# Optimization experiments

Hardware: AMD Instinct MI355X
Metric: run time of the kernel (lower is better)

Reference implementation:

```python
import jax, jax.numpy as jnp
import numpy as np

B, L, C, H = 4, 2048, 1024, 16
D = C // H  # head dim = 64


def setup_inputs() -> dict:
    key = jax.random.key(0)
    ks = jax.random.split(key, 7)
    x = jax.random.normal(ks[0], (B, L, C), dtype=jnp.float32)
    Wqkv = jax.random.normal(ks[1], (C, 3 * C), dtype=jnp.float32) * 0.02
    bqkv = jnp.zeros((3 * C,), dtype=jnp.float32)
    gamma_q = jnp.ones((H, D), dtype=jnp.float32)
    gamma_k = jnp.ones((H, D), dtype=jnp.float32)
    Wout = jax.random.normal(ks[2], (C, C), dtype=jnp.float32) * 0.02
    bout = jnp.zeros((C,), dtype=jnp.float32)
    return {"x": x, "Wqkv": Wqkv, "bqkv": bqkv, "gamma_q": gamma_q,
            "gamma_k": gamma_k, "Wout": Wout, "bout": bout}


def _multihead_rms_norm(t, gamma):
    # SparseMultiHeadRMSNorm: L2-normalize last dim (F.normalize), * gamma * sqrt(D)
    norm = jnp.maximum(jnp.linalg.norm(t, axis=-1, keepdims=True), 1e-12)
    return (t / norm) * gamma * jnp.sqrt(jnp.float32(D))


def reference(x, Wqkv, bqkv, gamma_q, gamma_k, Wout, bout):
    # qkv projection: [B,L,C] -> [B,L,3,H,D]
    qkv = (x @ Wqkv + bqkv).reshape(B, L, 3, H, D)
    q, k, v = qkv[:, :, 0], qkv[:, :, 1], qkv[:, :, 2]
    # qk rms norm (gamma broadcasts over [B,L,H,D])
    q = _multihead_rms_norm(q, gamma_q)
    k = _multihead_rms_norm(k, gamma_k)
    # full scaled dot product attention within each grid (batch element)
    scale = 1.0 / jnp.sqrt(jnp.float32(D))
    scores = jnp.einsum('bqhd,bkhd->bhqk', q, k) * scale
    attn = jax.nn.softmax(scores, axis=-1)
    h = jnp.einsum('bhqk,bkhd->bqhd', attn, v).reshape(B, L, C)
    return h @ Wout + bout
```

## Files before the change

### kernel.cpp

```cpp
#include <hip/hip_runtime.h>
#include <math.h>

#define BB 4
#define LL 2048
#define CC 1024
#define HH 16
#define DD 64
#define MM (BB * LL)

typedef float f32x4 __attribute__((ext_vector_type(4)));
typedef short short8 __attribute__((ext_vector_type(8)));
typedef unsigned short ushort_t;
typedef unsigned long long u64_t;

#define MFMA_BF16(A, B, C) __builtin_amdgcn_mfma_f32_16x16x32_bf16(A, B, C, 0, 0, 0)

#define QSCALE 0.180336880f

__device__ __forceinline__ unsigned short f2bf(float x) {
    unsigned int u = __float_as_uint(x);
    u += 0x7fffu + ((u >> 16) & 1u);
    return (unsigned short)(u >> 16);
}
__device__ __forceinline__ float bf2f(unsigned short h) {
    return __uint_as_float(((unsigned int)h) << 16);
}

__device__ __forceinline__ unsigned pack_bf2(float a, float b) {
#if __has_builtin(__builtin_amdgcn_perm)
    return __builtin_amdgcn_perm(__float_as_uint(b) + 0x8000u,
                                 __float_as_uint(a) + 0x8000u, 0x07060302u);
#else
    return ((__float_as_uint(b) + 0x8000u) & 0xFFFF0000u) |
           ((__float_as_uint(a) + 0x8000u) >> 16);
#endif
}

__device__ __forceinline__ float fast_exp2(float x) {
#if __has_builtin(__builtin_amdgcn_exp2f)
    return __builtin_amdgcn_exp2f(x);
#else
    return exp2f(x);
#endif
}

__global__ __launch_bounds__(256)
void round_bf16(const float* __restrict__ src, ushort_t* __restrict__ dst, int n)
{
    const int i = (blockIdx.x * 256 + threadIdx.x) * 8;
    if (i >= n) return;
    f32x4 a = *(const f32x4*)(src + i);
    f32x4 b = *(const f32x4*)(src + i + 4);
    short8 h;
#pragma unroll
    for (int j = 0; j < 4; ++j) {
        h[j]     = (short)f2bf(a[j]);
        h[4 + j] = (short)f2bf(b[j]);
    }
    *(short8*)(dst + i) = h;
}

__global__ __launch_bounds__(256)
void transp_hi(const float* __restrict__ W, ushort_t* __restrict__ Th,
               int K, int N)
{
    __shared__ float sT[64][65];
    const int k0 = blockIdx.y * 64, n0 = blockIdx.x * 64;
    const int tid = threadIdx.x;
    const int r = tid >> 2, c0 = (tid & 3) * 16;

    const float* wp = W + (size_t)(k0 + r) * N + n0 + c0;
#pragma unroll
    for (int u = 0; u < 4; ++u) {
        f32x4 v = *(const f32x4*)(wp + 4 * u);
        sT[r][c0 + 4 * u + 0] = v[0];
        sT[r][c0 + 4 * u + 1] = v[1];
        sT[r][c0 + 4 * u + 2] = v[2];
        sT[r][c0 + 4 * u + 3] = v[3];
    }
    __syncthreads();

    const int nn = tid >> 2, kk0 = (tid & 3) * 16;
    short8 h0, h1;
#pragma unroll
    for (int u = 0; u < 8; ++u) {
        h0[u] = (short)f2bf(sT[kk0 + u][nn]);
        h1[u] = (short)f2bf(sT[kk0 + 8 + u][nn]);
    }
    ushort_t* oh = Th + (size_t)(n0 + nn) * K + k0 + kk0;
    *(short8*)oh = h0; *(short8*)(oh + 8) = h1;
}

__global__ __launch_bounds__(256, 3)
void gemm_qkv(const ushort_t* __restrict__ Agh,
              const ushort_t* __restrict__ Bh,
              const float* __restrict__ bias,
              const float* __restrict__ gq, const float* __restrict__ gk,
              ushort_t* __restrict__ Qbh,
              ushort_t* __restrict__ Kh,
              ushort_t* __restrict__ Vth)
{
    __shared__ ushort_t smem[16384];
    ushort_t* sAh = smem;
    ushort_t* sBh = smem + 8192;

    const int K = CC, lda = CC, nbx = (3 * CC) / 128;

    const int nwg = gridDim.x;
    const int cpx = nwg >> 3;
    const int id  = blockIdx.x;
    const int swz = (id & 7) * cpx + (id >> 3);
    const int bx = swz % nbx, by = swz / nbx;
    const int m0 = by * 128, n0 = bx * 128;

    const int tid  = threadIdx.x;
    const int lane = tid & 63;
    const int wv   = tid >> 6;
    const int l4   = lane >> 4, l16 = lane & 15;
    const int wm   = wv >> 1,  wn  = wv & 1;

    const int r0  = tid >> 2;
    const int c0  = (tid & 3) * 16;
    const int ch0 = c0 >> 3;

    f32x4 acc[4][4];
#pragma unroll
    for (int i = 0; i < 4; ++i)
#pragma unroll
        for (int j = 0; j < 4; ++j) acc[i][j] = 0.f;

    for (int kt = 0; kt < K; kt += 64) {
        __syncthreads();
#pragma unroll
        for (int it = 0; it < 2; ++it) {
            const int row  = r0 + 64 * it;
            const int sA   = row & 7;
            const int base = row * 64;
            const int cA = ((ch0) ^ sA) * 8, cB = ((ch0 + 1) ^ sA) * 8;

            const ushort_t* ahp = Agh + (size_t)(m0 + row) * lda + kt + c0;
            *(short8*)&sAh[base + cA] = *(const short8*)(ahp);
            *(short8*)&sAh[base + cB] = *(const short8*)(ahp + 8);
            const ushort_t* bhp = Bh + (size_t)(n0 + row) * K + kt + c0;
            *(short8*)&sBh[base + cA] = *(const short8*)(bhp);
            *(short8*)&sBh[base + cB] = *(const short8*)(bhp + 8);
        }
        __syncthreads();

#pragma unroll
        for (int ks = 0; ks < 2; ++ks) {
            const int chf = (((ks << 2) | l4) ^ (l16 & 7)) * 8;
            short8 fbh[4];
#pragma unroll
            for (int j = 0; j < 4; ++j) {
                const int idx = (64 * wn + 16 * j + l16) * 64 + chf;
                fbh[j] = *(const short8*)&sBh[idx];
            }
#pragma unroll
            for (int i = 0; i < 4; ++i) {
                const int idx = (64 * wm + 16 * i + l16) * 64 + chf;
                short8 fah = *(const short8*)&sAh[idx];
#pragma unroll
                for (int j = 0; j < 4; ++j)
                    acc[i][j] = MFMA_BF16(fah, fbh[j], acc[i][j]);
            }
        }
    }

    const int region = n0 >> 10;
    float bv[4];
#pragma unroll
    for (int j = 0; j < 4; ++j) bv[j] = bias[n0 + 64 * wn + 16 * j + l16];
#pragma unroll
    for (int i = 0; i < 4; ++i)
#pragma unroll
        for (int j = 0; j < 4; ++j)
#pragma unroll
            for (int r = 0; r < 4; ++r) acc[i][j][r] += bv[j];

    const int b = m0 >> 11;

    if (region < 2) {
        const int hloc = ((n0 & 1023) >> 6) + wn;
        const float* g = (region == 0 ? gq : gk) + hloc * DD;
        float gv[4];
#pragma unroll
        for (int j = 0; j < 4; ++j) gv[j] = g[16 * j + l16];
#pragma unroll
        for (int i = 0; i < 4; ++i)
#pragma unroll
        for (int r = 0; r < 4; ++r) {
            float ss = 0.f;
#pragma unroll
            for (int j = 0; j < 4; ++j) ss += acc[i][j][r] * acc[i][j][r];
#pragma unroll
            for (int off = 1; off < 16; off <<= 1) ss += __shfl_xor(ss, off);
            const float s = 8.0f / fmaxf(sqrtf(ss), 1e-12f);
#pragma unroll
            for (int j = 0; j < 4; ++j) acc[i][j][r] *= s * gv[j];
        }

        if (region == 0) {
#pragma unroll
            for (int i = 0; i < 4; ++i)
#pragma unroll
            for (int r = 0; r < 4; ++r) {
                const int row = m0 + 64 * wm + 16 * i + 4 * l4 + r;
                ushort_t* op = Qbh + (size_t)row * CC + n0 + 64 * wn + l16;
#pragma unroll
                for (int j = 0; j < 4; ++j)
                    op[16 * j] = f2bf(acc[i][j][r] * QSCALE);
            }
        } else {
            const int hk = ((n0 - 1024) >> 6) + wn;
#pragma unroll
            for (int i = 0; i < 4; ++i)
#pragma unroll
            for (int r = 0; r < 4; ++r) {
                const int l = (m0 & 2047) + 64 * wm + 16 * i + 4 * l4 + r;
                const size_t base = ((size_t)(b * HH + hk) * LL + l) * DD + l16;
#pragma unroll
                for (int j = 0; j < 4; ++j)
                    Kh[base + 16 * j] = f2bf(acc[i][j][r]);
            }
        }
    } else {
        __syncthreads();
        ushort_t* vh = smem;
#pragma unroll
        for (int i = 0; i < 4; ++i)
#pragma unroll
        for (int r = 0; r < 4; ++r) {
            const int lr = 64 * wm + 16 * i + 4 * l4 + r;
#pragma unroll
            for (int j = 0; j < 4; ++j) {
                const int c = 64 * wn + 16 * j + l16;
                vh[lr * 128 + c] = f2bf(acc[i][j][r]);
            }
        }
        __syncthreads();
        const int c    = tid & 127;
        const int half = tid >> 7;
        const int hv   = ((n0 - 2048) >> 6) + (c >> 6);
        const int d    = c & 63;
        ushort_t* oh = Vth + ((size_t)(b * HH + hv) * DD + d) * LL + (m0 & 2047) + half * 64;
#pragma unroll
        for (int u = 0; u < 8; ++u) {
            const int l0 = half * 64 + u * 8;
            short8 hv8;
#pragma unroll
            for (int e = 0; e < 8; ++e)
                hv8[e] = (short)vh[(l0 + e) * 128 + c];
            *(short8*)&oh[u * 8] = hv8;
        }
    }
}

__global__ __launch_bounds__(256, 3)
void gemm_out1(const ushort_t* __restrict__ Ah,
               const ushort_t* __restrict__ Bh,
               const float* __restrict__ bias, float* __restrict__ Cg)
{
    __shared__ ushort_t sAh[8192];
    __shared__ ushort_t sBh[8192];

    const int K = CC, nbx = CC / 128;

    const int nwg = gridDim.x;
    const int cpx = nwg >> 3;
    const int id  = blockIdx.x;
    const int sw  = (id & 7) * cpx + (id >> 3);
    const int bx = sw % nbx, by = sw / nbx;
    const int m0 = by * 128, n0 = bx * 128;

    const int tid  = threadIdx.x;
    const int lane = tid & 63;
    const int wv   = tid >> 6;
    const int l4   = lane >> 4, l16 = lane & 15;
    const int wm   = wv >> 1,  wn  = wv & 1;

    const int r0  = tid >> 2;
    const int c0  = (tid & 3) * 16;
    const int ch0 = c0 >> 3;

    f32x4 acc[4][4];
#pragma unroll
    for (int i = 0; i < 4; ++i)
#pragma unroll
        for (int j = 0; j < 4; ++j) acc[i][j] = 0.f;

    for (int kt = 0; kt < K; kt += 64) {
        __syncthreads();
#pragma unroll
        for (int it = 0; it < 2; ++it) {
            const int row  = r0 + 64 * it;
            const int sA   = row & 7;
            const int base = row * 64;
            const int cA = ((ch0) ^ sA) * 8, cB = ((ch0 + 1) ^ sA) * 8;

            const ushort_t* ahp = Ah + (size_t)(m0 + row) * CC + kt + c0;
            *(short8*)&sAh[base + cA] = *(const short8*)(ahp);
            *(short8*)&sAh[base + cB] = *(const short8*)(ahp + 8);
            const ushort_t* bhp = Bh + (size_t)(n0 + row) * K + kt + c0;
            *(short8*)&sBh[base + cA] = *(const short8*)(bhp);
            *(short8*)&sBh[base + cB] = *(const short8*)(bhp + 8);
        }
        __syncthreads();

#pragma unroll
        for (int ks = 0; ks < 2; ++ks) {
            const int chf = (((ks << 2) | l4) ^ (l16 & 7)) * 8;
            short8 fbh[4];
#pragma unroll
            for (int j = 0; j < 4; ++j) {
                const int idx = (64 * wn + 16 * j + l16) * 64 + chf;
                fbh[j] = *(const short8*)&sBh[idx];
            }
#pragma unroll
            for (int i = 0; i < 4; ++i) {
                const int idx = (64 * wm + 16 * i + l16) * 64 + chf;
                short8 fah = *(const short8*)&sAh[idx];
#pragma unroll
                for (int j = 0; j < 4; ++j)
                    acc[i][j] = MFMA_BF16(fah, fbh[j], acc[i][j]);
            }
        }
    }

    float bv[4];
#pragma unroll
    for (int j = 0; j < 4; ++j) bv[j] = bias[n0 + 64 * wn + 16 * j + l16];
#pragma unroll
    for (int i = 0; i < 4; ++i)
#pragma unroll
    for (int r = 0; r < 4; ++r) {
        const int row = m0 + 64 * wm + 16 * i + 4 * l4 + r;
        float* cp = Cg + (size_t)row * CC + n0 + 64 * wn + l16;
#pragma unroll
        for (int j = 0; j < 4; ++j) cp[16 * j] = acc[i][j][r] + bv[j];
    }
}

__global__ __launch_bounds__(256, 3)
void flash9(const ushort_t* __restrict__ Qbh,
            const ushort_t* __restrict__ Kh,
            const ushort_t* __restrict__ Vth,
            ushort_t* __restrict__ Hb)
{
    __shared__ ushort_t sKh[4096], sVh[4096];
    __shared__ ushort_t sP[4][32 * 68];

    const int i    = blockIdx.x;
    const int xcd  = i & 7;
    const int slot = i >> 3;
    const int qt   = slot & 15;
    const int bh   = ((slot >> 4) << 3) | xcd;
    const int b    = bh >> 4, h = bh & 15;

    const int tid  = threadIdx.x;
    const int lane = tid & 63;
    const int wv   = tid >> 6;
    const int l4   = lane >> 4, l16 = lane & 15;

    short8 qh[2][2];
    const int qr0 = qt * 128 + wv * 32;
#pragma unroll
    for (int qf = 0; qf < 2; ++qf)
#pragma unroll
    for (int sl = 0; sl < 2; ++sl)
        qh[qf][sl] = *(const short8*)(Qbh + (size_t)(b * LL + qr0 + qf * 16 + l16) * CC
                                      + h * DD + sl * 32 + l4 * 8);

    short8 ones;
#pragma unroll
    for (int j = 0; j < 8; ++j) ones[j] = (short)0x3F80;

    f32x4 O[2][4];
    f32x4 acc_l[2];
#pragma unroll
    for (int qf = 0; qf < 2; ++qf) {
        acc_l[qf] = 0.f;
#pragma unroll
        for (int t = 0; t < 4; ++t) O[qf][t] = 0.f;
    }

    const int r_ = tid >> 2;
    const int c2 = (tid & 3) * 2;

    short8 stg[4];
    {
        const size_t kgb = ((size_t)bh * LL + r_) * DD + c2 * 8;
        const size_t vgb = ((size_t)bh * DD + r_) * LL + c2 * 8;
        stg[0] = *(const short8*)&Kh[kgb];  stg[1] = *(const short8*)&Kh[kgb + 8];
        stg[2] = *(const short8*)&Vth[vgb]; stg[3] = *(const short8*)&Vth[vgb + 8];
    }

    for (int kt = 0; kt < LL / 64; ++kt) {
        __syncthreads();
        {
            const int wr = r_ * 64, s = r_ & 7;
            const int cA = ((c2) ^ s) * 8, cB = ((c2 + 1) ^ s) * 8;
            *(short8*)&sKh[wr + cA] = stg[0];
            *(short8*)&sKh[wr + cB] = stg[1];
            *(short8*)&sVh[wr + cA] = stg[2];
            *(short8*)&sVh[wr + cB] = stg[3];
        }
        __syncthreads();
        if (kt + 1 < LL / 64) {
            const size_t kgb = ((size_t)bh * LL + (kt + 1) * 64 + r_) * DD + c2 * 8;
            const size_t vgb = ((size_t)bh * DD + r_) * LL + (kt + 1) * 64 + c2 * 8;
            stg[0] = *(const short8*)&Kh[kgb];  stg[1] = *(const short8*)&Kh[kgb + 8];
            stg[2] = *(const short8*)&Vth[vgb]; stg[3] = *(const short8*)&Vth[vgb + 8];
        }

        f32x4 S[2][4];
#pragma unroll
        for (int qf = 0; qf < 2; ++qf)
#pragma unroll
        for (int t = 0; t < 4; ++t) S[qf][t] = 0.f;

        __builtin_amdgcn_s_setprio(1);
#pragma unroll
        for (int t = 0; t < 4; ++t) {
            const int row = 16 * t + l16;
            const int swr = row & 7;
#pragma unroll
            for (int sl = 0; sl < 2; ++sl) {
                const int idx = row * 64 + (((sl << 2) | l4) ^ swr) * 8;
                short8 kh8 = *(const short8*)&sKh[idx];
#pragma unroll
                for (int qf = 0; qf < 2; ++qf)
                    S[qf][t] = MFMA_BF16(kh8, qh[qf][sl], S[qf][t]);
            }
        }
        __builtin_amdgcn_s_setprio(0);

#pragma unroll
        for (int qf = 0; qf < 2; ++qf)
#pragma unroll
        for (int t = 0; t < 4; ++t)
#pragma unroll
            for (int r = 0; r < 4; ++r)
                S[qf][t][r] = fast_exp2(S[qf][t][r]);

#pragma unroll
        for (int qf = 0; qf < 2; ++qf)
#pragma unroll
        for (int t = 0; t < 4; ++t) {
            unsigned lo = pack_bf2(S[qf][t][0], S[qf][t][1]);
            unsigned hi = pack_bf2(S[qf][t][2], S[qf][t][3]);
            const int widx = (qf * 16 + l16) * 68 + 16 * t + 4 * l4;
            *(u64_t*)&sP[wv][widx] = (u64_t)lo | ((u64_t)hi << 32);
        }
        asm volatile("s_waitcnt lgkmcnt(0)" ::: "memory");
        __builtin_amdgcn_sched_barrier(0);

        short8 pa[2][2];
#pragma unroll
        for (int qf = 0; qf < 2; ++qf)
#pragma unroll
        for (int sl = 0; sl < 2; ++sl) {
            const int ridx = (qf * 16 + l16) * 68 + sl * 32 + 8 * l4;
            union { u64_t q[2]; short8 s8; } u;
            u.q[0] = *(const u64_t*)&sP[wv][ridx];
            u.q[1] = *(const u64_t*)&sP[wv][ridx + 4];
            pa[qf][sl] = u.s8;
        }

        __builtin_amdgcn_s_setprio(1);
#pragma unroll
        for (int qf = 0; qf < 2; ++qf) {
            acc_l[qf] = MFMA_BF16(pa[qf][0], ones, acc_l[qf]);
            acc_l[qf] = MFMA_BF16(pa[qf][1], ones, acc_l[qf]);
        }
#pragma unroll
        for (int dt = 0; dt < 4; ++dt) {
            const int row = 16 * dt + l16;
            const int swr = row & 7;
#pragma unroll
            for (int sl = 0; sl < 2; ++sl) {
                const int idx = row * 64 + (((sl << 2) | l4) ^ swr) * 8;
                short8 vh8 = *(const short8*)&sVh[idx];
#pragma unroll
                for (int qf = 0; qf < 2; ++qf)
                    O[qf][dt] = MFMA_BF16(pa[qf][sl], vh8, O[qf][dt]);
            }
        }
        __builtin_amdgcn_s_setprio(0);
    }

#pragma unroll
    for (int qf = 0; qf < 2; ++qf) {
        f32x4 iv;
#pragma unroll
        for (int r = 0; r < 4; ++r) iv[r] = 1.0f / acc_l[qf][r];
#pragma unroll
        for (int r = 0; r < 4; ++r) {
            const int q = qr0 + qf * 16 + 4 * l4 + r;
            ushort_t* op = Hb + (size_t)(b * LL + q) * CC + h * DD + l16;
#pragma unroll
            for (int dt = 0; dt < 4; ++dt)
                op[16 * dt] = f2bf(O[qf][dt][r] * iv[r]);
        }
    }
}

#define Bb 128
#define Bn 128
#define BKG 8

__global__ __launch_bounds__(256)
void gemm_bias(const float* __restrict__ A, const float* __restrict__ B,
               const float* __restrict__ bias, float* __restrict__ C,
               int M, int N, int K, int lda, int ldb, int ldc)
{
    __shared__ float As[BKG][Bb];
    __shared__ float Bs[BKG][Bn];

    const int tid = threadIdx.x;
    const int m0 = blockIdx.y * Bb;
    const int n0 = blockIdx.x * Bn;
    const int ty = tid >> 4, tx = tid & 15;
    const int arow = tid >> 1, acol = (tid & 1) * 4;
    const int brow = tid >> 5, bcol = (tid & 31) * 4;

    const float* Ap = A + (size_t)(m0 + arow) * lda + acol;
    const float* Bp = B + (size_t)brow * ldb + n0 + bcol;

    float acc[8][8];
#pragma unroll
    for (int i = 0; i < 8; ++i)
#pragma unroll
        for (int j = 0; j < 8; ++j) acc[i][j] = 0.f;

    for (int k0 = 0; k0 < K; k0 += BKG) {
        float4 av = *(const float4*)(Ap + k0);
        float4 bv = *(const float4*)(Bp + (size_t)k0 * ldb);
        __syncthreads();
        As[acol + 0][arow] = av.x;
        As[acol + 1][arow] = av.y;
        As[acol + 2][arow] = av.z;
        As[acol + 3][arow] = av.w;
        *(float4*)&Bs[brow][bcol] = bv;
        __syncthreads();
#pragma unroll
        for (int kk = 0; kk < BKG; ++kk) {
            float a[8], bvv[8];
            *(float4*)&a[0] = *(const float4*)&As[kk][ty * 4];
            *(float4*)&a[4] = *(const float4*)&As[kk][64 + ty * 4];
            *(float4*)&bvv[0] = *(const float4*)&Bs[kk][tx * 4];
            *(float4*)&bvv[4] = *(const float4*)&Bs[kk][64 + tx * 4];
#pragma unroll
            for (int i = 0; i < 8; ++i)
#pragma unroll
                for (int j = 0; j < 8; ++j)
                    acc[i][j] = fmaf(a[i], bvv[j], acc[i][j]);
        }
    }
#pragma unroll
    for (int ih = 0; ih < 2; ++ih)
#pragma unroll
    for (int i = 0; i < 4; ++i) {
        const int m = m0 + ih * 64 + ty * 4 + i;
#pragma unroll
        for (int jh = 0; jh < 2; ++jh) {
            const int n = n0 + jh * 64 + tx * 4;
            float4 o;
            o.x = acc[ih*4+i][jh*4+0] + bias[n+0];
            o.y = acc[ih*4+i][jh*4+1] + bias[n+1];
            o.z = acc[ih*4+i][jh*4+2] + bias[n+2];
            o.w = acc[ih*4+i][jh*4+3] + bias[n+3];
            *(float4*)(C + (size_t)m * ldc + n) = o;
        }
    }
}

__global__ __launch_bounds__(256)
void rmsnorm_qk(float* __restrict__ qkv,
                const float* __restrict__ gq, const float* __restrict__ gk)
{
    const int gt    = blockIdx.x * 256 + threadIdx.x;
    const int lane  = gt & 63;
    const int wave  = gt >> 6;
    const int which = wave & 1;
    const int h     = (wave >> 1) & (HH - 1);
    const int bl    = wave >> 5;

    float* p = qkv + (size_t)bl * (3 * CC) + which * CC + h * DD + lane;
    float v = *p;
    float ss = v * v;
#pragma unroll
    for (int off = 32; off; off >>= 1) ss += __shfl_xor(ss, off);
    float nrm = fmaxf(sqrtf(ss), 1e-12f);
    const float* g = which ? gk : gq;
    *p = v * (8.0f / nrm) * g[h * DD + lane];
}

__global__ __launch_bounds__(256)
void flash_fp32(float* __restrict__ qkv)
{
    const int qt = blockIdx.x, hh = blockIdx.y, bb = blockIdx.z;

    __shared__ float Qt[DD][64];
    __shared__ float Kt[DD][64];
    __shared__ float Vs[64][DD];
    __shared__ float Ps[64][64 + 4];

    const int tid = threadIdx.x;
    const int ty = tid >> 4, tx = tid & 15;
    const size_t rs_ = 3 * CC;
    const float* qbase = qkv + ((size_t)bb * LL + (size_t)qt * 64) * rs_ + hh * DD;
    const float* kbase = qkv + (size_t)bb * LL * rs_ + CC + hh * DD;
    const float* vbase = kbase + CC;

    {
        const int r = tid >> 2, c0 = (tid & 3) * 16;
#pragma unroll
        for (int u = 0; u < 4; ++u) {
            float4 v = *(const float4*)(qbase + (size_t)r * rs_ + c0 + u * 4);
            Qt[c0 + u*4 + 0][r] = v.x; Qt[c0 + u*4 + 1][r] = v.y;
            Qt[c0 + u*4 + 2][r] = v.z; Qt[c0 + u*4 + 3][r] = v.w;
        }
    }

    float mrow[4], lrow[4], O[4][4];
#pragma unroll
    for (int i = 0; i < 4; ++i) {
        mrow[i] = -INFINITY; lrow[i] = 0.f;
#pragma unroll
        for (int j = 0; j < 4; ++j) O[i][j] = 0.f;
    }

    for (int kt = 0; kt < LL / 64; ++kt) {
        __syncthreads();
        {
            const int r = tid >> 2, c0 = (tid & 3) * 16;
            const float* kr = kbase + ((size_t)kt * 64 + r) * rs_;
            const float* vr = vbase + ((size_t)kt * 64 + r) * rs_;
#pragma unroll
            for (int u = 0; u < 4; ++u) {
                float4 kv = *(const float4*)(kr + c0 + u * 4);
                Kt[c0 + u*4 + 0][r] = kv.x; Kt[c0 + u*4 + 1][r] = kv.y;
                Kt[c0 + u*4 + 2][r] = kv.z; Kt[c0 + u*4 + 3][r] = kv.w;
                *(float4*)&Vs[r][c0 + u*4] = *(const float4*)(vr + c0 + u * 4);
            }
        }
        __syncthreads();

        float S[4][4];
#pragma unroll
        for (int i = 0; i < 4; ++i)
#pragma unroll
            for (int j = 0; j < 4; ++j) S[i][j] = 0.f;
#pragma unroll 8
        for (int d = 0; d < DD; ++d) {
            float a[4], b[4];
            *(float4*)a = *(const float4*)&Qt[d][ty * 4];
            *(float4*)b = *(const float4*)&Kt[d][tx * 4];
#pragma unroll
            for (int i = 0; i < 4; ++i)
#pragma unroll
                for (int j = 0; j < 4; ++j) S[i][j] = fmaf(a[i], b[j], S[i][j]);
        }
#pragma unroll
        for (int i = 0; i < 4; ++i) {
#pragma unroll
            for (int j = 0; j < 4; ++j) S[i][j] *= 0.125f;
            float pm = fmaxf(fmaxf(S[i][0], S[i][1]), fmaxf(S[i][2], S[i][3]));
#pragma unroll
            for (int off = 1; off < 16; off <<= 1) pm = fmaxf(pm, __shfl_xor(pm, off));
            const float mnew = fmaxf(mrow[i], pm);
            const float corr = __expf(mrow[i] - mnew);
            float rsum = 0.f;
#pragma unroll
            for (int j = 0; j < 4; ++j) { S[i][j] = __expf(S[i][j] - mnew); rsum += S[i][j]; }
#pragma unroll
            for (int off = 1; off < 16; off <<= 1) rsum += __shfl_xor(rsum, off);
            mrow[i] = mnew;
            lrow[i] = lrow[i] * corr + rsum;
#pragma unroll
            for (int j = 0; j < 4; ++j) O[i][j] *= corr;
        }
#pragma unroll
        for (int i = 0; i < 4; ++i)
            *(float4*)&Ps[ty * 4 + i][tx * 4] = *(float4*)&S[i][0];
        __syncthreads();
#pragma unroll 4
        for (int k = 0; k < 64; k += 4) {
            float a[4][4];
#pragma unroll
            for (int i = 0; i < 4; ++i)
                *(float4*)&a[i][0] = *(const float4*)&Ps[ty * 4 + i][k];
#pragma unroll
            for (int kk = 0; kk < 4; ++kk) {
                float bv[4];
                *(float4*)bv = *(const float4*)&Vs[k + kk][tx * 4];
#pragma unroll
                for (int i = 0; i < 4; ++i)
#pragma unroll
                    for (int j = 0; j < 4; ++j)
                        O[i][j] = fmaf(a[i][kk], bv[j], O[i][j]);
            }
        }
    }

    float* obase = qkv + ((size_t)bb * LL + (size_t)qt * 64) * rs_ + hh * DD;
#pragma unroll
    for (int i = 0; i < 4; ++i) {
        const float inv = 1.f / lrow[i];
        float4 o;
        o.x = O[i][0] * inv; o.y = O[i][1] * inv;
        o.z = O[i][2] * inv; o.w = O[i][3] * inv;
        *(float4*)(obase + (size_t)(ty * 4 + i) * rs_ + tx * 4) = o;
    }
}

extern "C" void kernel_launch(void* const* d_in, const int* in_sizes, int n_in,
                              void* d_out, int out_size, void* d_ws, size_t ws_size,
                              hipStream_t stream)
{
    const float* x    = (const float*)d_in[0];
    const float* Wqkv = (const float*)d_in[1];
    const float* bqkv = (const float*)d_in[2];
    const float* gq   = (const float*)d_in[3];
    const float* gk   = (const float*)d_in[4];
    const float* Wout = (const float*)d_in[5];
    const float* bout = (const float*)d_in[6];
    float* out = (float*)d_out;

    const size_t NEED = 92274688ull;

    if (ws_size >= NEED) {
        char* wsb = (char*)d_ws;
        ushort_t* Qbh = (ushort_t*)(wsb);
        ushort_t* Kh  = (ushort_t*)(wsb + 16777216);
        ushort_t* Vth = (ushort_t*)(wsb + 33554432);
        ushort_t* Hb  = (ushort_t*)(wsb + 50331648);
        ushort_t* wqh = (ushort_t*)(wsb + 67108864);
        ushort_t* woh = (ushort_t*)(wsb + 73400320);
        ushort_t* xh  = (ushort_t*)(wsb + 75497472);

        transp_hi<<<dim3(3 * CC / 64, CC / 64), 256, 0, stream>>>(Wqkv, wqh, CC, 3 * CC);
        transp_hi<<<dim3(CC / 64, CC / 64), 256, 0, stream>>>(Wout, woh, CC, CC);
        round_bf16<<<dim3(MM * CC / 8 / 256), 256, 0, stream>>>(x, xh, MM * CC);

        gemm_qkv<<<dim3(24 * 64), 256, 0, stream>>>(
            xh, wqh, bqkv, gq, gk, Qbh, Kh, Vth);

        flash9<<<dim3(1024), 256, 0, stream>>>(Qbh, Kh, Vth, Hb);

        gemm_out1<<<dim3(8 * 64), 256, 0, stream>>>(Hb, woh, bout, out);
    } else {
        float* qkv = (float*)d_ws;
        gemm_bias<<<dim3((3 * CC) / Bn, MM / Bb), 256, 0, stream>>>(
            x, Wqkv, bqkv, qkv, MM, 3 * CC, CC, CC, 3 * CC, 3 * CC);
        rmsnorm_qk<<<dim3((MM * HH * 2 * 64) / 256), 256, 0, stream>>>(qkv, gq, gk);
        flash_fp32<<<dim3(LL / 64, HH, BB), 256, 0, stream>>>(qkv);
        gemm_bias<<<dim3(CC / Bn, MM / Bb), 256, 0, stream>>>(
            qkv, Wout, bout, out, MM, CC, CC, 3 * CC, CC, CC);
    }
}
```

Measured before the change: 193.1 us.

## Fuse x bf16 rounding into QKV GEMM and widen flash K/V tiles

Removes the separate round_bf16 pass by having the QKV GEMM load fp32 x and convert it to bf16 while staging into shared memory. This avoids writing and rereading a 16MB bf16 copy, but x is now reread in fp32 by every column tile. Separately, the attention kernel now stages 128-key K/V tiles per barrier pair instead of 64, with wider swizzles for V. The larger shared-memory footprint and staging registers lower the occupancy hint from 3 to 2 blocks.

```diff
diff --git a/kernel.cpp b/kernel.cpp
--- a/kernel.cpp
+++ b/kernel.cpp
@@ -45,22 +45,6 @@
 }
 
 __global__ __launch_bounds__(256)
-void round_bf16(const float* __restrict__ src, ushort_t* __restrict__ dst, int n)
-{
-    const int i = (blockIdx.x * 256 + threadIdx.x) * 8;
-    if (i >= n) return;
-    f32x4 a = *(const f32x4*)(src + i);
-    f32x4 b = *(const f32x4*)(src + i + 4);
-    short8 h;
-#pragma unroll
-    for (int j = 0; j < 4; ++j) {
-        h[j]     = (short)f2bf(a[j]);
-        h[4 + j] = (short)f2bf(b[j]);
-    }
-    *(short8*)(dst + i) = h;
-}
-
-__global__ __launch_bounds__(256)
 void transp_hi(const float* __restrict__ W, ushort_t* __restrict__ Th,
                int K, int N)
 {
@@ -92,7 +76,7 @@
 }
 
 __global__ __launch_bounds__(256, 3)
-void gemm_qkv(const ushort_t* __restrict__ Agh,
+void gemm_qkv(const float* __restrict__ X,
               const ushort_t* __restrict__ Bh,
               const float* __restrict__ bias,
               const float* __restrict__ gq, const float* __restrict__ gk,
@@ -104,7 +88,7 @@
     ushort_t* sAh = smem;
     ushort_t* sBh = smem + 8192;
 
-    const int K = CC, lda = CC, nbx = (3 * CC) / 128;
+    const int K = CC, nbx = (3 * CC) / 128;
 
     const int nwg = gridDim.x;
     const int cpx = nwg >> 3;
@@ -138,9 +122,21 @@
             const int base = row * 64;
             const int cA = ((ch0) ^ sA) * 8, cB = ((ch0 + 1) ^ sA) * 8;
 
-            const ushort_t* ahp = Agh + (size_t)(m0 + row) * lda + kt + c0;
-            *(short8*)&sAh[base + cA] = *(const short8*)(ahp);
-            *(short8*)&sAh[base + cB] = *(const short8*)(ahp + 8);
+            const float* ap = X + (size_t)(m0 + row) * CC + kt + c0;
+            f32x4 v0 = *(const f32x4*)(ap);
+            f32x4 v1 = *(const f32x4*)(ap + 4);
+            f32x4 v2 = *(const f32x4*)(ap + 8);
+            f32x4 v3 = *(const f32x4*)(ap + 12);
+            short8 h0, h1;
+#pragma unroll
+            for (int j = 0; j < 4; ++j) {
+                h0[j]     = (short)f2bf(v0[j]);
+                h0[4 + j] = (short)f2bf(v1[j]);
+                h1[j]     = (short)f2bf(v2[j]);
+                h1[4 + j] = (short)f2bf(v3[j]);
+            }
+            *(short8*)&sAh[base + cA] = h0;
+            *(short8*)&sAh[base + cB] = h1;
             const ushort_t* bhp = Bh + (size_t)(n0 + row) * K + kt + c0;
             *(short8*)&sBh[base + cA] = *(const short8*)(bhp);
             *(short8*)&sBh[base + cB] = *(const short8*)(bhp + 8);
@@ -341,13 +337,14 @@
     }
 }
 
-__global__ __launch_bounds__(256, 3)
-void flash9(const ushort_t* __restrict__ Qbh,
-            const ushort_t* __restrict__ Kh,
-            const ushort_t* __restrict__ Vth,
-            ushort_t* __restrict__ Hb)
+__global__ __launch_bounds__(256, 2)
+void flash10(const ushort_t* __restrict__ Qbh,
+             const ushort_t* __restrict__ Kh,
+             const ushort_t* __restrict__ Vth,
+             ushort_t* __restrict__ Hb)
 {
-    __shared__ ushort_t sKh[4096], sVh[4096];
+    __shared__ ushort_t sKh[128 * 64];
+    __shared__ ushort_t sVh[64 * 128];
     __shared__ ushort_t sP[4][32 * 68];
 
     const int i    = blockIdx.x;
@@ -384,109 +381,119 @@
         for (int t = 0; t < 4; ++t) O[qf][t] = 0.f;
     }
 
-    const int r_ = tid >> 2;
-    const int c2 = (tid & 3) * 2;
-
-    short8 stg[4];
+    const int rk = tid >> 1,  ck = (tid & 1) * 32;
+    const int rv = tid >> 2,  cv = (tid & 3) * 32;
+
+    short8 stg[8];
     {
-        const size_t kgb = ((size_t)bh * LL + r_) * DD + c2 * 8;
-        const size_t vgb = ((size_t)bh * DD + r_) * LL + c2 * 8;
-        stg[0] = *(const short8*)&Kh[kgb];  stg[1] = *(const short8*)&Kh[kgb + 8];
-        stg[2] = *(const short8*)&Vth[vgb]; stg[3] = *(const short8*)&Vth[vgb + 8];
-    }
-
-    for (int kt = 0; kt < LL / 64; ++kt) {
+        const size_t kgb = ((size_t)bh * LL + rk) * DD + ck;
+        const size_t vgb = ((size_t)bh * DD + rv) * LL + cv;
+#pragma unroll
+        for (int u = 0; u < 4; ++u) {
+            stg[u]     = *(const short8*)&Kh[kgb + 8 * u];
+            stg[4 + u] = *(const short8*)&Vth[vgb + 8 * u];
+        }
+    }
+
+    for (int kt = 0; kt < LL / 128; ++kt) {
         __syncthreads();
         {
-            const int wr = r_ * 64, s = r_ & 7;
-            const int cA = ((c2) ^ s) * 8, cB = ((c2 + 1) ^ s) * 8;
-            *(short8*)&sKh[wr + cA] = stg[0];
-            *(short8*)&sKh[wr + cB] = stg[1];
-            *(short8*)&sVh[wr + cA] = stg[2];
-            *(short8*)&sVh[wr + cB] = stg[3];
-        }
-        __syncthreads();
-        if (kt + 1 < LL / 64) {
-            const size_t kgb = ((size_t)bh * LL + (kt + 1) * 64 + r_) * DD + c2 * 8;
-            const size_t vgb = ((size_t)bh * DD + r_) * LL + (kt + 1) * 64 + c2 * 8;
-            stg[0] = *(const short8*)&Kh[kgb];  stg[1] = *(const short8*)&Kh[kgb + 8];
-            stg[2] = *(const short8*)&Vth[vgb]; stg[3] = *(const short8*)&Vth[vgb + 8];
-        }
-
-        f32x4 S[2][4];
-#pragma unroll
-        for (int qf = 0; qf < 2; ++qf)
-#pragma unroll
-        for (int t = 0; t < 4; ++t) S[qf][t] = 0.f;
-
-        __builtin_amdgcn_s_setprio(1);
-#pragma unroll
-        for (int t = 0; t < 4; ++t) {
-            const int row = 16 * t + l16;
-            const int swr = row & 7;
+            const int kbase = rk * 64, ksw = rk & 7;
+            const int vbase = rv * 128, vsw = rv & 15;
+#pragma unroll
+            for (int u = 0; u < 4; ++u) {
+                *(short8*)&sKh[kbase + (((ck >> 3) + u) ^ ksw) * 8] = stg[u];
+                *(short8*)&sVh[vbase + (((cv >> 3) + u) ^ vsw) * 8] = stg[4 + u];
+            }
+        }
+        __syncthreads();
+        if (kt + 1 < LL / 128) {
+            const size_t kgb = ((size_t)bh * LL + (kt + 1) * 128 + rk) * DD + ck;
+            const size_t vgb = ((size_t)bh * DD + rv) * LL + (kt + 1) * 128 + cv;
+#pragma unroll
+            for (int u = 0; u < 4; ++u) {
+                stg[u]     = *(const short8*)&Kh[kgb + 8 * u];
+                stg[4 + u] = *(const short8*)&Vth[vgb + 8 * u];
+            }
+        }
+
+#pragma unroll
+        for (int kh = 0; kh < 2; ++kh) {
+            f32x4 S[2][4];
+#pragma unroll
+            for (int qf = 0; qf < 2; ++qf)
+#pragma unroll
+            for (int t = 0; t < 4; ++t) S[qf][t] = 0.f;
+
+            __builtin_amdgcn_s_setprio(1);
+#pragma unroll
+            for (int t = 0; t < 4; ++t) {
+                const int row = 64 * kh + 16 * t + l16;
+                const int swr = row & 7;
+#pragma unroll
+                for (int sl = 0; sl < 2; ++sl) {
+                    const int idx = row * 64 + (((sl << 2) | l4) ^ swr) * 8;
+                    short8 kh8 = *(const short8*)&sKh[idx];
+#pragma unroll
+                    for (int qf = 0; qf < 2; ++qf)
+                        S[qf][t] = MFMA_BF16(kh8, qh[qf][sl], S[qf][t]);
+                }
+            }
+            __builtin_amdgcn_s_setprio(0);
+
+#pragma unroll
+            for (int qf = 0; qf < 2; ++qf)
+#pragma unroll
+            for (int t = 0; t < 4; ++t)
+#pragma unroll
+                for (int r = 0; r < 4; ++r)
+                    S[qf][t][r] = fast_exp2(S[qf][t][r]);
+
+#pragma unroll
+            for (int qf = 0; qf < 2; ++qf)
+#pragma unroll
+            for (int t = 0; t < 4; ++t) {
+                unsigned lo = pack_bf2(S[qf][t][0], S[qf][t][1]);
+                unsigned hi = pack_bf2(S[qf][t][2], S[qf][t][3]);
+                const int widx = (qf * 16 + l16) * 68 + 16 * t + 4 * l4;
+                *(u64_t*)&sP[wv][widx] = (u64_t)lo | ((u64_t)hi << 32);
+            }
+            asm volatile("s_waitcnt lgkmcnt(0)" ::: "memory");
+            __builtin_amdgcn_sched_barrier(0);
+
+            short8 pa[2][2];
+#pragma unroll
+            for (int qf = 0; qf < 2; ++qf)
 #pragma unroll
             for (int sl = 0; sl < 2; ++sl) {
-                const int idx = row * 64 + (((sl << 2) | l4) ^ swr) * 8;
-                short8 kh8 = *(const short8*)&sKh[idx];
-#pragma unroll
-                for (int qf = 0; qf < 2; ++qf)
-                    S[qf][t] = MFMA_BF16(kh8, qh[qf][sl], S[qf][t]);
-            }
-        }
-        __builtin_amdgcn_s_setprio(0);
-
-#pragma unroll
-        for (int qf = 0; qf < 2; ++qf)
-#pragma unroll
-        for (int t = 0; t < 4; ++t)
-#pragma unroll
-            for (int r = 0; r < 4; ++r)
-                S[qf][t][r] = fast_exp2(S[qf][t][r]);
-
-#pragma unroll
-        for (int qf = 0; qf < 2; ++qf)
-#pragma unroll
-        for (int t = 0; t < 4; ++t) {
-            unsigned lo = pack_bf2(S[qf][t][0], S[qf][t][1]);
-            unsigned hi = pack_bf2(S[qf][t][2], S[qf][t][3]);
-            const int widx = (qf * 16 + l16) * 68 + 16 * t + 4 * l4;
-            *(u64_t*)&sP[wv][widx] = (u64_t)lo | ((u64_t)hi << 32);
-        }
-        asm volatile("s_waitcnt lgkmcnt(0)" ::: "memory");
-        __builtin_amdgcn_sched_barrier(0);
-
-        short8 pa[2][2];
-#pragma unroll
-        for (int qf = 0; qf < 2; ++qf)
-#pragma unroll
-        for (int sl = 0; sl < 2; ++sl) {
-            const int ridx = (qf * 16 + l16) * 68 + sl * 32 + 8 * l4;
-            union { u64_t q[2]; short8 s8; } u;
-            u.q[0] = *(const u64_t*)&sP[wv][ridx];
-            u.q[1] = *(const u64_t*)&sP[wv][ridx + 4];
-            pa[qf][sl] = u.s8;
-        }
-
-        __builtin_amdgcn_s_setprio(1);
-#pragma unroll
-        for (int qf = 0; qf < 2; ++qf) {
-            acc_l[qf] = MFMA_BF16(pa[qf][0], ones, acc_l[qf]);
-            acc_l[qf] = MFMA_BF16(pa[qf][1], ones, acc_l[qf]);
-        }
-#pragma unroll
-        for (int dt = 0; dt < 4; ++dt) {
-            const int row = 16 * dt + l16;
-            const int swr = row & 7;
-#pragma unroll
-            for (int sl = 0; sl < 2; ++sl) {
-                const int idx = row * 64 + (((sl << 2) | l4) ^ swr) * 8;
-                short8 vh8 = *(const short8*)&sVh[idx];
-#pragma unroll
-                for (int qf = 0; qf < 2; ++qf)
-                    O[qf][dt] = MFMA_BF16(pa[qf][sl], vh8, O[qf][dt]);
-            }
-        }
-        __builtin_amdgcn_s_setprio(0);
+                const int ridx = (qf * 16 + l16) * 68 + sl * 32 + 8 * l4;
+                union { u64_t q[2]; short8 s8; } u;
+                u.q[0] = *(const u64_t*)&sP[wv][ridx];
+                u.q[1] = *(const u64_t*)&sP[wv][ridx + 4];
+                pa[qf][sl] = u.s8;
+            }
+
+            __builtin_amdgcn_s_setprio(1);
+#pragma unroll
+            for (int qf = 0; qf < 2; ++qf) {
+                acc_l[qf] = MFMA_BF16(pa[qf][0], ones, acc_l[qf]);
+                acc_l[qf] = MFMA_BF16(pa[qf][1], ones, acc_l[qf]);
+            }
+#pragma unroll
+            for (int dt = 0; dt < 4; ++dt) {
+                const int row = 16 * dt + l16;
+                const int swv = row & 15;
+#pragma unroll
+                for (int sl = 0; sl < 2; ++sl) {
+                    const int idx = row * 128 + (((kh << 3) | (sl << 2) | l4) ^ swv) * 8;
+                    short8 vh8 = *(const short8*)&sVh[idx];
+#pragma unroll
+                    for (int qf = 0; qf < 2; ++qf)
+                        O[qf][dt] = MFMA_BF16(pa[qf][sl], vh8, O[qf][dt]);
+                }
+            }
+            __builtin_amdgcn_s_setprio(0);
+        }
     }
 
 #pragma unroll
@@ -728,7 +735,7 @@
     const float* bout = (const float*)d_in[6];
     float* out = (float*)d_out;
 
-    const size_t NEED = 92274688ull;
+    const size_t NEED = 75497472ull;
 
     if (ws_size >= NEED) {
         char* wsb = (char*)d_ws;
@@ -738,16 +745,14 @@
         ushort_t* Hb  = (ushort_t*)(wsb + 50331648);
         ushort_t* wqh = (ushort_t*)(wsb + 67108864);
         ushort_t* woh = (ushort_t*)(wsb + 73400320);
-        ushort_t* xh  = (ushort_t*)(wsb + 75497472);
 
         transp_hi<<<dim3(3 * CC / 64, CC / 64), 256, 0, stream>>>(Wqkv, wqh, CC, 3 * CC);
         transp_hi<<<dim3(CC / 64, CC / 64), 256, 0, stream>>>(Wout, woh, CC, CC);
-        round_bf16<<<dim3(MM * CC / 8 / 256), 256, 0, stream>>>(x, xh, MM * CC);
 
         gemm_qkv<<<dim3(24 * 64), 256, 0, stream>>>(
-            xh, wqh, bqkv, gq, gk, Qbh, Kh, Vth);
-
-        flash9<<<dim3(1024), 256, 0, stream>>>(Qbh, Kh, Vth, Hb);
+            x, wqh, bqkv, gq, gk, Qbh, Kh, Vth);
+
+        flash10<<<dim3(1024), 256, 0, stream>>>(Qbh, Kh, Vth, Hb);
 
         gemm_out1<<<dim3(8 * 64), 256, 0, stream>>>(Hb, woh, bout, out);
     } else {
```

Measured after the change: 224.1 us. 1.16x slower.

## Fuse prep kernels into one launch and register-prefetch next GEMM tiles

Applied to the files above, without the earlier changes.

Merges the x-to-bf16 rounding and the two weight transpose kernels into a single prep_all launch, dispatching on block index, which removes two kernel launches and their gaps. Both bf16 GEMMs (QKV and output) now prefetch the next K-tile from global memory into registers while the current tile's MFMAs run, so global load latency overlaps compute. The prefetch costs extra VGPRs per thread, which may lower occupancy under the existing launch bounds.

```diff
diff --git a/kernel.cpp b/kernel.cpp
--- a/kernel.cpp
+++ b/kernel.cpp
@@ -21,9 +21,6 @@
     unsigned int u = __float_as_uint(x);
     u += 0x7fffu + ((u >> 16) & 1u);
     return (unsigned short)(u >> 16);
-}
-__device__ __forceinline__ float bf2f(unsigned short h) {
-    return __uint_as_float(((unsigned int)h) << 16);
 }
 
 __device__ __forceinline__ unsigned pack_bf2(float a, float b) {
@@ -45,28 +42,37 @@
 }
 
 __global__ __launch_bounds__(256)
-void round_bf16(const float* __restrict__ src, ushort_t* __restrict__ dst, int n)
-{
-    const int i = (blockIdx.x * 256 + threadIdx.x) * 8;
-    if (i >= n) return;
-    f32x4 a = *(const f32x4*)(src + i);
-    f32x4 b = *(const f32x4*)(src + i + 4);
-    short8 h;
-#pragma unroll
-    for (int j = 0; j < 4; ++j) {
-        h[j]     = (short)f2bf(a[j]);
-        h[4 + j] = (short)f2bf(b[j]);
-    }
-    *(short8*)(dst + i) = h;
-}
-
-__global__ __launch_bounds__(256)
-void transp_hi(const float* __restrict__ W, ushort_t* __restrict__ Th,
-               int K, int N)
+void prep_all(const float* __restrict__ x, ushort_t* __restrict__ xh,
+              const float* __restrict__ Wq, ushort_t* __restrict__ Tq,
+              const float* __restrict__ Wo, ushort_t* __restrict__ To)
 {
     __shared__ float sT[64][65];
-    const int k0 = blockIdx.y * 64, n0 = blockIdx.x * 64;
+    int bid = blockIdx.x;
     const int tid = threadIdx.x;
+
+    if (bid < 4096) {
+        const int i = (bid * 256 + tid) * 8;
+        f32x4 a = *(const f32x4*)(x + i);
+        f32x4 b = *(const f32x4*)(x + i + 4);
+        short8 h;
+#pragma unroll
+        for (int j = 0; j < 4; ++j) {
+            h[j]     = (short)f2bf(a[j]);
+            h[4 + j] = (short)f2bf(b[j]);
+        }
+        *(short8*)(xh + i) = h;
+        return;
+    }
+    bid -= 4096;
+
+    const float* W;
+    ushort_t* T;
+    int N, bx, by;
+    if (bid < 768) { W = Wq; T = Tq; N = 3 * CC; bx = bid % 48; by = bid / 48; }
+    else { bid -= 768; W = Wo; T = To; N = CC; bx = bid % 16; by = bid / 16; }
+
+    const int K = CC;
+    const int k0 = by * 64, n0 = bx * 64;
     const int r = tid >> 2, c0 = (tid & 3) * 16;
 
     const float* wp = W + (size_t)(k0 + r) * N + n0 + c0;
@@ -87,7 +93,7 @@
         h0[u] = (short)f2bf(sT[kk0 + u][nn]);
         h1[u] = (short)f2bf(sT[kk0 + 8 + u][nn]);
     }
-    ushort_t* oh = Th + (size_t)(n0 + nn) * K + k0 + kk0;
+    ushort_t* oh = T + (size_t)(n0 + nn) * K + k0 + kk0;
     *(short8*)oh = h0; *(short8*)(oh + 8) = h1;
 }
 
@@ -129,6 +135,17 @@
 #pragma unroll
         for (int j = 0; j < 4; ++j) acc[i][j] = 0.f;
 
+    short8 stgA[4], stgB[4];
+#pragma unroll
+    for (int it = 0; it < 2; ++it) {
+        const ushort_t* ahp = Agh + (size_t)(m0 + r0 + 64 * it) * lda + c0;
+        stgA[2 * it]     = *(const short8*)(ahp);
+        stgA[2 * it + 1] = *(const short8*)(ahp + 8);
+        const ushort_t* bhp = Bh + (size_t)(n0 + r0 + 64 * it) * K + c0;
+        stgB[2 * it]     = *(const short8*)(bhp);
+        stgB[2 * it + 1] = *(const short8*)(bhp + 8);
+    }
+
     for (int kt = 0; kt < K; kt += 64) {
         __syncthreads();
 #pragma unroll
@@ -137,15 +154,24 @@
             const int sA   = row & 7;
             const int base = row * 64;
             const int cA = ((ch0) ^ sA) * 8, cB = ((ch0 + 1) ^ sA) * 8;
-
-            const ushort_t* ahp = Agh + (size_t)(m0 + row) * lda + kt + c0;
-            *(short8*)&sAh[base + cA] = *(const short8*)(ahp);
-            *(short8*)&sAh[base + cB] = *(const short8*)(ahp + 8);
-            const ushort_t* bhp = Bh + (size_t)(n0 + row) * K + kt + c0;
-            *(short8*)&sBh[base + cA] = *(const short8*)(bhp);
-            *(short8*)&sBh[base + cB] = *(const short8*)(bhp + 8);
-        }
-        __syncthreads();
+            *(short8*)&sAh[base + cA] = stgA[2 * it];
+            *(short8*)&sAh[base + cB] = stgA[2 * it + 1];
+            *(short8*)&sBh[base + cA] = stgB[2 * it];
+            *(short8*)&sBh[base + cB] = stgB[2 * it + 1];
+        }
+        __syncthreads();
+
+        if (kt + 64 < K) {
+#pragma unroll
+            for (int it = 0; it < 2; ++it) {
+                const ushort_t* ahp = Agh + (size_t)(m0 + r0 + 64 * it) * lda + kt + 64 + c0;
+                stgA[2 * it]     = *(const short8*)(ahp);
+                stgA[2 * it + 1] = *(const short8*)(ahp + 8);
+                const ushort_t* bhp = Bh + (size_t)(n0 + r0 + 64 * it) * K + kt + 64 + c0;
+                stgB[2 * it]     = *(const short8*)(bhp);
+                stgB[2 * it + 1] = *(const short8*)(bhp + 8);
+            }
+        }
 
 #pragma unroll
         for (int ks = 0; ks < 2; ++ks) {
@@ -289,6 +315,17 @@
 #pragma unroll
         for (int j = 0; j < 4; ++j) acc[i][j] = 0.f;
 
+    short8 stgA[4], stgB[4];
+#pragma unroll
+    for (int it = 0; it < 2; ++it) {
+        const ushort_t* ahp = Ah + (size_t)(m0 + r0 + 64 * it) * CC + c0;
+        stgA[2 * it]     = *(const short8*)(ahp);
+        stgA[2 * it + 1] = *(const short8*)(ahp + 8);
+        const ushort_t* bhp = Bh + (size_t)(n0 + r0 + 64 * it) * K + c0;
+        stgB[2 * it]     = *(const short8*)(bhp);
+        stgB[2 * it + 1] = *(const short8*)(bhp + 8);
+    }
+
     for (int kt = 0; kt < K; kt += 64) {
         __syncthreads();
 #pragma unroll
@@ -297,15 +334,24 @@
             const int sA   = row & 7;
             const int base = row * 64;
             const int cA = ((ch0) ^ sA) * 8, cB = ((ch0 + 1) ^ sA) * 8;
-
-            const ushort_t* ahp = Ah + (size_t)(m0 + row) * CC + kt + c0;
-            *(short8*)&sAh[base + cA] = *(const short8*)(ahp);
-            *(short8*)&sAh[base + cB] = *(const short8*)(ahp + 8);
-            const ushort_t* bhp = Bh + (size_t)(n0 + row) * K + kt + c0;
-            *(short8*)&sBh[base + cA] = *(const short8*)(bhp);
-            *(short8*)&sBh[base + cB] = *(const short8*)(bhp + 8);
-        }
-        __syncthreads();
+            *(short8*)&sAh[base + cA] = stgA[2 * it];
+            *(short8*)&sAh[base + cB] = stgA[2 * it + 1];
+            *(short8*)&sBh[base + cA] = stgB[2 * it];
+            *(short8*)&sBh[base + cB] = stgB[2 * it + 1];
+        }
+        __syncthreads();
+
+        if (kt + 64 < K) {
+#pragma unroll
+            for (int it = 0; it < 2; ++it) {
+                const ushort_t* ahp = Ah + (size_t)(m0 + r0 + 64 * it) * CC + kt + 64 + c0;
+                stgA[2 * it]     = *(const short8*)(ahp);
+                stgA[2 * it + 1] = *(const short8*)(ahp + 8);
+                const ushort_t* bhp = Bh + (size_t)(n0 + r0 + 64 * it) * K + kt + 64 + c0;
+                stgB[2 * it]     = *(const short8*)(bhp);
+                stgB[2 * it + 1] = *(const short8*)(bhp + 8);
+            }
+        }
 
 #pragma unroll
         for (int ks = 0; ks < 2; ++ks) {
@@ -740,9 +786,8 @@
         ushort_t* woh = (ushort_t*)(wsb + 73400320);
         ushort_t* xh  = (ushort_t*)(wsb + 75497472);
 
-        transp_hi<<<dim3(3 * CC / 64, CC / 64), 256, 0, stream>>>(Wqkv, wqh, CC, 3 * CC);
-        transp_hi<<<dim3(CC / 64, CC / 64), 256, 0, stream>>>(Wout, woh, CC, CC);
-        round_bf16<<<dim3(MM * CC / 8 / 256), 256, 0, stream>>>(x, xh, MM * CC);
+        prep_all<<<dim3(4096 + 768 + 256), 256, 0, stream>>>(
+            x, xh, Wqkv, wqh, Wout, woh);
 
         gemm_qkv<<<dim3(24 * 64), 256, 0, stream>>>(
             xh, wqh, bqkv, gq, gk, Qbh, Kh, Vth);
```

Measured after the change: 193.4 us. About the same (+0.1%).
